# Optimization experiments

Measured on AMD Instinct MI355X. Metric: run time of the kernel, lower is better.

Reference implementation:

```python
import jax, jax.numpy as jnp
import numpy as np

N_NODES = 50000
N_EDGES = 800000
N_GRAPHS = 512
F_IN = 9
U = 64  # model_units


def _add_self_loops(edge_index, n):
    loop = jnp.arange(n, dtype=edge_index.dtype)
    return jnp.concatenate([edge_index, jnp.stack([loop, loop])], axis=1)


def gat_conv(x, edge_index, W, a_src, a_dst, b):
    # PyG GATConv, heads=1, negative_slope=0.2, add_self_loops=True
    n = x.shape[0]
    ei = _add_self_loops(edge_index, n)
    src, dst = ei[0], ei[1]
    h = x @ W                              # [n, U]
    alpha_s = h @ a_src                    # [n]
    alpha_d = h @ a_dst                    # [n]
    e = jax.nn.leaky_relu(alpha_s[src] + alpha_d[dst], 0.2)   # [E+n]
    m = jax.ops.segment_max(e, dst, num_segments=n)           # stable softmax over incoming edges
    ex = jnp.exp(e - m[dst])
    denom = jax.ops.segment_sum(ex, dst, num_segments=n)
    coef = ex / denom[dst]                 # [E+n]
    out = jax.ops.segment_sum(h[src] * coef[:, None], dst, num_segments=n)
    return out + b


def gcn_conv(x, edge_index, W, b):
    # PyG GCNConv with symmetric normalization and self loops
    n = x.shape[0]
    ei = _add_self_loops(edge_index, n)
    src, dst = ei[0], ei[1]
    h = x @ W                              # [n, U]
    deg = jax.ops.segment_sum(jnp.ones(src.shape, h.dtype), dst, num_segments=n)
    dinv = jnp.where(deg > 0, jax.lax.rsqrt(deg), 0.0)
    norm = dinv[src] * dinv[dst]           # [E+n]
    out = jax.ops.segment_sum(h[src] * norm[:, None], dst, num_segments=n)
    return out + b


def _branch(x, edge_index, W_gat, a_src, a_dst, b_gat, W_gcn, b_gcn, W1, b1, W2, b2, W3, b3):
    x = jnp.tanh(gat_conv(x, edge_index, W_gat, a_src, a_dst, b_gat))
    for i in range(W_gcn.shape[0]):        # model_layers - 1 = 2 GCN layers
        x = jnp.tanh(gcn_conv(x, edge_index, W_gcn[i], b_gcn[i]))
        # dropout is a no-op in eval mode
    x = jnp.tanh(x @ W1 + b1)
    x = jnp.tanh(x @ W2 + b2)
    x = x @ W3 + b3                        # [n, 1]; dropout no-op in eval
    return x


def _mean_pool(x, batch, num_graphs):
    sums = jax.ops.segment_sum(x, batch, num_segments=num_graphs)
    cnt = jax.ops.segment_sum(jnp.ones((x.shape[0],), x.dtype), batch, num_segments=num_graphs)
    return sums / jnp.maximum(cnt, 1.0)[:, None]


def setup_inputs() -> dict:
    key = jax.random.key(0)
    ks = jax.random.split(key, 16)
    inp = {
        "x_a": jax.random.normal(ks[0], (N_NODES, F_IN), jnp.float32),
        "x_b": jax.random.normal(ks[1], (N_NODES, F_IN), jnp.float32),
        "edge_index_a": jax.random.randint(ks[2], (2, N_EDGES), 0, N_NODES, jnp.int32),
        "edge_index_b": jax.random.randint(ks[3], (2, N_EDGES), 0, N_NODES, jnp.int32),
        "batch_a": jnp.sort(jax.random.randint(ks[4], (N_NODES,), 0, N_GRAPHS, jnp.int32)),
        "batch_b": jnp.sort(jax.random.randint(ks[5], (N_NODES,), 0, N_GRAPHS, jnp.int32)),
        # parameters
        "W_gat": jax.random.normal(ks[6], (F_IN, U), jnp.float32) * 0.3,
        "a_src": jax.random.normal(ks[7], (U,), jnp.float32) * 0.3,
        "a_dst": jax.random.normal(ks[8], (U,), jnp.float32) * 0.3,
        "b_gat": jnp.zeros((U,), jnp.float32),
        "W_gcn": jax.random.normal(ks[9], (2, U, U), jnp.float32) * (1.0 / np.sqrt(U)),
        "b_gcn": jnp.zeros((2, U), jnp.float32),
        "W1": jax.random.normal(ks[10], (U, U), jnp.float32) * (1.0 / np.sqrt(U)),
        "b1": jnp.zeros((U,), jnp.float32),
        "W2": jax.random.normal(ks[11], (U, 32), jnp.float32) * (1.0 / np.sqrt(U)),
        "b2": jnp.zeros((32,), jnp.float32),
        "W3": jax.random.normal(ks[12], (32, 1), jnp.float32) * (1.0 / np.sqrt(32.0)),
        "b3": jnp.zeros((1,), jnp.float32),
    }
    return inp


def reference(x_a, x_b, edge_index_a, edge_index_b, batch_a, batch_b,
              W_gat, a_src, a_dst, b_gat, W_gcn, b_gcn, W1, b1, W2, b2, W3, b3):
    params = (W_gat, a_src, a_dst, b_gat, W_gcn, b_gcn, W1, b1, W2, b2, W3, b3)
    ha = _branch(x_a, edge_index_a, *params)
    hb = _branch(x_b, edge_index_b, *params)
    ua = _mean_pool(ha, batch_a, N_GRAPHS)   # [G, 1]
    ub = _mean_pool(hb, batch_b, N_GRAPHS)
    return jax.nn.sigmoid(ub - ua)
```

## Files before the change

### kernel.cpp

```cpp
#include <hip/hip_runtime.h>
#include <hip/hip_fp16.h>
#include <math.h>

#define NN 50000
#define NE 800000
#define NG 512
#define NET (NE + NN)
#define NT2 ((2 * NN + 63) / 64)
#define GN4 ((2 * NN + 3) / 4)
#define GN8 ((2 * NN + 7) / 8)
#define GN32 ((2 * NN + 31) / 32)
#define NSH 68

#define SLICE 512
#define NSL ((NN + SLICE - 1) / SLICE)
#define CHK 4096
#define NCK ((NET + CHK - 1) / CHK)
#define CAP 10240

typedef unsigned short u16;

__device__ __forceinline__ float wsum64(float v) {
#pragma unroll
    for (int o = 32; o > 0; o >>= 1) v += __shfl_down(v, o, 64);
    return v;
}

__device__ __forceinline__ float fast_tanh(float x) {
    return 1.f - 2.f / (__expf(2.f * x) + 1.f);
}


__global__ __launch_bounds__(256) void k_hist(const int* __restrict__ eia,
                                              const int* __restrict__ eib,
                                              int* __restrict__ cnts) {
    __shared__ int h[NSL];
    int b = blockIdx.x;
    int br = b >= NCK, c = b - (br ? NCK : 0);
    int t = threadIdx.x;
    for (int i = t; i < NSL; i += 256) h[i] = 0;
    __syncthreads();
    const int* ei = br ? eib : eia;
    int e0 = c * CHK, e1 = e0 + CHK; if (e1 > NET) e1 = NET;
    for (int e = e0 + t; e < e1; e += 256) {
        int d = (e < NE) ? __builtin_nontemporal_load(&ei[NE + e]) : (e - NE);
        atomicAdd(&h[d >> 9], 1);
    }
    __syncthreads();
    for (int i = t; i < NSL; i += 256) cnts[(br * NSL + i) * NCK + c] = h[i];
}

__global__ __launch_bounds__(64) void k_off1(int* __restrict__ cnts,
                                             int* __restrict__ sliceBase) {
    int b = blockIdx.x;
    int br = b >= NSL, s = b - (br ? NSL : 0);
    int lane = threadIdx.x;
    int* row = cnts + (br * NSL + s) * NCK;
    int run = 0;
    for (int c0 = 0; c0 < NCK; c0 += 64) {
        int c = c0 + lane;
        int v = (c < NCK) ? row[c] : 0;
        int orig = v;
#pragma unroll
        for (int o = 1; o < 64; o <<= 1) {
            int tv = __shfl_up(v, o, 64);
            if (lane >= o) v += tv;
        }
        if (c < NCK) row[c] = run + v - orig;
        run += __shfl(v, 63, 64);
    }
    if (lane == 0) sliceBase[br * (NSL + 1) + s] = run;
}

__global__ void k_off2(int* __restrict__ sliceBase, int* __restrict__ rowptr2,
                       float* __restrict__ pool) {
    int t = threadIdx.x;
    for (int i = t; i < 4 * NG; i += 256) pool[i] = 0.f;
    if (t < 2) {
        int* sb = sliceBase + t * (NSL + 1);
        int run = 0;
        for (int s = 0; s < NSL; s++) { int v = sb[s]; sb[s] = run; run += v; }
        sb[NSL] = run;
        rowptr2[t * (NN + 1) + NN] = run;
    }
}

__global__ __launch_bounds__(256) void k_bucket(const int* __restrict__ eia,
                                                const int* __restrict__ eib,
                                                const int* __restrict__ cnts,
                                                const int* __restrict__ sliceBase,
                                                unsigned int* __restrict__ staging) {
    __shared__ int cur[NSL];
    int b = blockIdx.x;
    int br = b >= NCK, c = b - (br ? NCK : 0);
    int t = threadIdx.x;
    for (int i = t; i < NSL; i += 256)
        cur[i] = cnts[(br * NSL + i) * NCK + c] + sliceBase[br * (NSL + 1) + i];
    __syncthreads();
    const int* ei = br ? eib : eia;
    unsigned int* stg = staging + (size_t)br * NET;
    int e0 = c * CHK, e1 = e0 + CHK; if (e1 > NET) e1 = NET;
    for (int e = e0 + t; e < e1; e += 256) {
        int d, s;
        if (e < NE) {
            d = __builtin_nontemporal_load(&ei[NE + e]);
            s = __builtin_nontemporal_load(&ei[e]);
        } else { d = e - NE; s = d; }
        int pos = atomicAdd(&cur[d >> 9], 1);
        stg[pos] = ((unsigned int)(d & 511) << 16) | (unsigned int)s;
    }
}

__global__ __launch_bounds__(512) void k_slice(const unsigned int* __restrict__ staging,
                                               const int* __restrict__ sliceBase,
                                               int* __restrict__ rowptr2,
                                               float* __restrict__ dinv2,
                                               u16* __restrict__ csr2) {
    __shared__ int sc[512];
    __shared__ int cur[512];
    __shared__ u16 buf[CAP];
    int b = blockIdx.x;
    int br = b >= NSL, sl = b - (br ? NSL : 0);
    int t = threadIdx.x;
    const int* sb = sliceBase + br * (NSL + 1);
    int base = sb[sl], m = sb[sl + 1] - base;
    const unsigned int* st = staging + (size_t)br * NET + base;
    cur[t] = 0;
    __syncthreads();
    for (int i = t; i < m; i += 512) atomicAdd(&cur[st[i] >> 16], 1);
    __syncthreads();
    int v = cur[t];
    sc[t] = v;
    __syncthreads();
    for (int o = 1; o < 512; o <<= 1) {
        int add = (t >= o) ? sc[t - o] : 0;
        __syncthreads();
        sc[t] += add;
        __syncthreads();
    }
    int excl = sc[t] - v;
    int node = sl * SLICE + t;
    if (node < NN) {
        rowptr2[br * (NN + 1) + node] = base + excl;
        dinv2[br * NN + node] = v > 0 ? rsqrtf((float)v) : 0.f;
    }
    cur[t] = excl;
    __syncthreads();
    for (int i = t; i < m; i += 512) {
        unsigned int e = st[i];
        int pos = atomicAdd(&cur[e >> 16], 1);
        if (pos < CAP) buf[pos] = (u16)(e & 0xffffu);
    }
    __syncthreads();
    u16* out = csr2 + (size_t)br * NET + base;
    int mm = m < CAP ? m : CAP;
    for (int i = t; i < mm; i += 512) out[i] = buf[i];
}

__global__ __launch_bounds__(256) void k_wprep(const float* __restrict__ W1,
                                               const float* __restrict__ W2,
                                               const float* __restrict__ Wgcn,
                                               __half* __restrict__ out) {
    int i = blockIdx.x * 256 + threadIdx.x;
    float v;
    if (i < 4096) v = W1[i];
    else if (i < 6144) v = W2[i - 4096];
    else v = Wgcn[i - 6144];
    out[i] = __float2half(v);
}


__global__ void k_gat_input(const float* __restrict__ xa, const float* __restrict__ xb,
                            const float* __restrict__ Wg,
                            const float* __restrict__ avs, const float* __restrict__ avd,
                            __half* __restrict__ A, float* __restrict__ als,
                            float* __restrict__ ald) {
    __shared__ float sW[9 * 64];
    __shared__ float sas[64], sad[64];
    int t = threadIdx.x;
    for (int i = t; i < 9 * 64; i += 256) sW[i] = Wg[i];
    if (t < 64) { sas[t] = avs[t]; sad[t] = avd[t]; }
    __syncthreads();
    int n = blockIdx.x * 4 + (t >> 6);
    int u = t & 63;
    if (n >= 2 * NN) return;
    const float* xp = (n < NN) ? &xa[(size_t)n * 9] : &xb[(size_t)(n - NN) * 9];
    float h = 0.f;
#pragma unroll
    for (int f = 0; f < 9; f++) h += xp[f] * sW[f * 64 + u];
    A[(size_t)n * 64 + u] = __float2half(h);
    float ps = wsum64(h * sas[u]);
    float pd = wsum64(h * sad[u]);
    if (u == 0) { als[n] = ps; ald[n] = pd; }
}

__global__ __launch_bounds__(256) void k_edgew(
        const int* __restrict__ rowptr2, const u16* __restrict__ csr2,
        const float* __restrict__ als, const float* __restrict__ ald,
        float* __restrict__ wn) {
    int u = threadIdx.x & 63;
    int lu = u & 31;
    int dg = blockIdx.x * 8 + (threadIdx.x >> 6) * 2 + (u >> 5);
    if (dg >= 2 * NN) return;
    int br = dg >= NN;
    int d = dg - br * NN;
    const int* rp = rowptr2 + br * (NN + 1);
    const u16* cs = csr2 + br * NET;
    float* wp = wn + (size_t)br * NET;
    int nb = br * NN;
    int beg = rp[d], end = rp[d + 1];
    float ad = ald[dg];
    float den = 0.f;
    for (int c = beg + lu; c < end; c += 32) {
        int s = nb + cs[c];
        float v = als[s] + ad;
        float w = __expf(fmaxf(v, 0.2f * v));
        den += w;
        wp[c] = w;
    }
#pragma unroll
    for (int o = 16; o > 0; o >>= 1) den += __shfl_down(den, o, 32);
    den = __shfl(den, 0, 32);
    float inv = 1.f / den;
    for (int c = beg + lu; c < end; c += 32) wp[c] *= inv;
}

__device__ __forceinline__ void fma8(float* acc, float4 f, float w) {
    const __half2* h = (const __half2*)&f;
#pragma unroll
    for (int p = 0; p < 4; p++) {
        float2 v = __half22float2(h[p]);
        acc[2 * p]     += v.x * w;
        acc[2 * p + 1] += v.y * w;
    }
}

__global__ __launch_bounds__(256) void k_gat_gather8(
        const int* __restrict__ rowptr2, const u16* __restrict__ csr2,
        const float* __restrict__ wn, const __half* __restrict__ A,
        const float* __restrict__ bias, __half* __restrict__ B) {
    int lane = threadIdx.x & 63;
    int grp = lane >> 3, li = lane & 7;
    int dg = blockIdx.x * 32 + (threadIdx.x >> 6) * 8 + grp;
    int br = dg >= NN;
    int d = dg - br * NN;
    const int* rp = rowptr2 + br * (NN + 1);
    const u16* cs = csr2 + br * NET;
    const float* wp = wn + (size_t)br * NET;
    int nb = br * NN;
    int beg = rp[d], end = rp[d + 1];
    const float4* Af = (const float4*)A;
    float acc[8];
#pragma unroll
    for (int k = 0; k < 8; k++) acc[k] = 0.f;
    for (int j = beg; j < end; j += 4) {
        int i0 = j, i1 = j + 1, i2 = j + 2, i3 = j + 3;
        int c1 = i1 < end ? i1 : end - 1;
        int c2 = i2 < end ? i2 : end - 1;
        int c3 = i3 < end ? i3 : end - 1;
        float w0 = wp[i0];
        float w1 = i1 < end ? wp[c1] : 0.f;
        float w2 = i2 < end ? wp[c2] : 0.f;
        float w3 = i3 < end ? wp[c3] : 0.f;
        int s0 = nb + cs[i0];
        int s1 = nb + cs[c1];
        int s2 = nb + cs[c2];
        int s3 = nb + cs[c3];
        float4 f0 = Af[(size_t)s0 * 8 + li];
        float4 f1 = Af[(size_t)s1 * 8 + li];
        float4 f2 = Af[(size_t)s2 * 8 + li];
        float4 f3 = Af[(size_t)s3 * 8 + li];
        fma8(acc, f0, w0);
        fma8(acc, f1, w1);
        fma8(acc, f2, w2);
        fma8(acc, f3, w3);
    }
    const float4* bf = (const float4*)bias;
    float4 b0 = bf[2 * li], b1 = bf[2 * li + 1];
    __half2 o[4];
    o[0] = __floats2half2_rn(fast_tanh(acc[0] + b0.x), fast_tanh(acc[1] + b0.y));
    o[1] = __floats2half2_rn(fast_tanh(acc[2] + b0.z), fast_tanh(acc[3] + b0.w));
    o[2] = __floats2half2_rn(fast_tanh(acc[4] + b1.x), fast_tanh(acc[5] + b1.y));
    o[3] = __floats2half2_rn(fast_tanh(acc[6] + b1.z), fast_tanh(acc[7] + b1.w));
    ((float4*)B)[(size_t)dg * 8 + li] = *(float4*)o;
}

__global__ __launch_bounds__(256) void k_gcn_gather8(
        const int* __restrict__ rowptr2, const u16* __restrict__ csr2,
        const float* __restrict__ dinv, const __half* __restrict__ Y,
        const float* __restrict__ bias, __half* __restrict__ Bout) {
    int lane = threadIdx.x & 63;
    int grp = lane >> 3, li = lane & 7;
    int dg = blockIdx.x * 32 + (threadIdx.x >> 6) * 8 + grp;
    int br = dg >= NN;
    int d = dg - br * NN;
    const int* rp = rowptr2 + br * (NN + 1);
    const u16* cs = csr2 + br * NET;
    int nb = br * NN;
    int beg = rp[d], end = rp[d + 1];
    const float4* Yf = (const float4*)Y;
    float acc[8];
#pragma unroll
    for (int k = 0; k < 8; k++) acc[k] = 0.f;
    for (int j = beg; j < end; j += 4) {
        int i1 = j + 1, i2 = j + 2, i3 = j + 3;
        int c1 = i1 < end ? i1 : end - 1;
        int c2 = i2 < end ? i2 : end - 1;
        int c3 = i3 < end ? i3 : end - 1;
        float w1 = i1 < end ? 1.f : 0.f;
        float w2 = i2 < end ? 1.f : 0.f;
        float w3 = i3 < end ? 1.f : 0.f;
        int s0 = nb + cs[j];
        int s1 = nb + cs[c1];
        int s2 = nb + cs[c2];
        int s3 = nb + cs[c3];
        float4 f0 = Yf[(size_t)s0 * 8 + li];
        float4 f1 = Yf[(size_t)s1 * 8 + li];
        float4 f2 = Yf[(size_t)s2 * 8 + li];
        float4 f3 = Yf[(size_t)s3 * 8 + li];
        fma8(acc, f0, 1.f);
        fma8(acc, f1, w1);
        fma8(acc, f2, w2);
        fma8(acc, f3, w3);
    }
    float dv = dinv[dg];
    const float4* bf = (const float4*)bias;
    float4 b0 = bf[2 * li], b1 = bf[2 * li + 1];
    __half2 o[4];
    o[0] = __floats2half2_rn(fast_tanh(acc[0] * dv + b0.x), fast_tanh(acc[1] * dv + b0.y));
    o[1] = __floats2half2_rn(fast_tanh(acc[2] * dv + b0.z), fast_tanh(acc[3] * dv + b0.w));
    o[2] = __floats2half2_rn(fast_tanh(acc[4] * dv + b1.x), fast_tanh(acc[5] * dv + b1.y));
    o[3] = __floats2half2_rn(fast_tanh(acc[6] * dv + b1.z), fast_tanh(acc[7] * dv + b1.w));
    ((float4*)Bout)[(size_t)dg * 8 + li] = *(float4*)o;
}

__device__ __forceinline__ void load_tile_FM16(const __half* __restrict__ X, int base,
                                               __half* sXh, int t) {
    const float4* Xf = (const float4*)X;
#pragma unroll
    for (int rep = 0; rep < 2; rep++) {
        int i = t + rep * 256;
        int node = i >> 3, q = i & 7;
        float4 raw;
        if (base + node < 2 * NN) raw = Xf[(size_t)(base + node) * 8 + q];
        else raw = make_float4(0.f, 0.f, 0.f, 0.f);
        const __half* hv = (const __half*)&raw;
#pragma unroll
        for (int e = 0; e < 8; e++) sXh[(8 * q + e) * NSH + node] = hv[e];
    }
}

__global__ __launch_bounds__(256) void k_lin_tile(
        const __half* __restrict__ X, const __half* __restrict__ Wh,
        const float* __restrict__ dinv, __half* __restrict__ Y) {
    __shared__ __half sW[64 * 64];
    __shared__ __half sXh[64 * NSH];
    int t = threadIdx.x;
    {
        const uint4* src = (const uint4*)Wh;
        uint4* dst = (uint4*)sW;
        for (int i = t; i < 512; i += 256) dst[i] = src[i];
    }
    int base = blockIdx.x * 64;
    load_tile_FM16(X, base, sXh, t);
    __syncthreads();
    int tx = t & 15, ty = t >> 4;
    float acc[4][4];
#pragma unroll
    for (int i = 0; i < 4; i++)
#pragma unroll
        for (int j = 0; j < 4; j++) acc[i][j] = 0.f;
#pragma unroll 4
    for (int k = 0; k < 64; k++) {
        uint2 wraw = *(const uint2*)&sW[k * 64 + 4 * tx];
        float2 wa = __half22float2(*(__half2*)&wraw.x);
        float2 wb = __half22float2(*(__half2*)&wraw.y);
        uint2 xraw = *(const uint2*)&sXh[k * NSH + 4 * ty];
        float2 xa = __half22float2(*(__half2*)&xraw.x);
        float2 xb = __half22float2(*(__half2*)&xraw.y);
        acc[0][0] += xa.x * wa.x; acc[0][1] += xa.x * wa.y; acc[0][2] += xa.x * wb.x; acc[0][3] += xa.x * wb.y;
        acc[1][0] += xa.y * wa.x; acc[1][1] += xa.y * wa.y; acc[1][2] += xa.y * wb.x; acc[1][3] += xa.y * wb.y;
        acc[2][0] += xb.x * wa.x; acc[2][1] += xb.x * wa.y; acc[2][2] += xb.x * wb.x; acc[2][3] += xb.x * wb.y;
        acc[3][0] += xb.y * wa.x; acc[3][1] += xb.y * wa.y; acc[3][2] += xb.y * wb.x; acc[3][3] += xb.y * wb.y;
    }
#pragma unroll
    for (int i = 0; i < 4; i++) {
        int n = base + 4 * ty + i;
        if (n < 2 * NN) {
            float dv = dinv[n];
            __half2* Y2 = (__half2*)&Y[(size_t)n * 64 + 4 * tx];
            Y2[0] = __floats2half2_rn(acc[i][0] * dv, acc[i][1] * dv);
            Y2[1] = __floats2half2_rn(acc[i][2] * dv, acc[i][3] * dv);
        }
    }
}

__global__ __launch_bounds__(256) void k_mlp_pool(
        const __half* __restrict__ X,
        const int* __restrict__ batch_a, const int* __restrict__ batch_b,
        const __half* __restrict__ W1h, const float* __restrict__ b1,
        const __half* __restrict__ W2h, const float* __restrict__ b2,
        const float* __restrict__ W3, const float* __restrict__ b3,
        float* __restrict__ pool) {
    __shared__ __half sW1[64 * 64];
    __shared__ __half sW2[64 * 32];
    __shared__ __half sXh[64 * NSH];
    __shared__ float sP[64 * 9];
    __shared__ float sW3[32], sb1[64], sb2[32];
    __shared__ int sKey[64];
    __shared__ float sVal[64];
    int t = threadIdx.x;
    {
        const uint4* s1 = (const uint4*)W1h;
        uint4* d1 = (uint4*)sW1;
        for (int i = t; i < 512; i += 256) d1[i] = s1[i];
        const uint4* s2 = (const uint4*)W2h;
        uint4* d2 = (uint4*)sW2;
        if (t < 256) d2[t] = s2[t];
    }
    if (t < 64) sb1[t] = b1[t];
    if (t < 32) { sW3[t] = W3[t]; sb2[t] = b2[t]; }
    float bb3 = b3[0];
    int base = blockIdx.x * 64;
    load_tile_FM16(X, base, sXh, t);
    __syncthreads();
    int tx = t & 15, ty = t >> 4;
    float acc[4][4];
#pragma unroll
    for (int i = 0; i < 4; i++)
#pragma unroll
        for (int j = 0; j < 4; j++) acc[i][j] = sb1[4 * tx + j];
#pragma unroll 4
    for (int k = 0; k < 64; k++) {
        uint2 wraw = *(const uint2*)&sW1[k * 64 + 4 * tx];
        float2 wa = __half22float2(*(__half2*)&wraw.x);
        float2 wb = __half22float2(*(__half2*)&wraw.y);
        uint2 xraw = *(const uint2*)&sXh[k * NSH + 4 * ty];
        float2 xa = __half22float2(*(__half2*)&xraw.x);
        float2 xb = __half22float2(*(__half2*)&xraw.y);
        acc[0][0] += xa.x * wa.x; acc[0][1] += xa.x * wa.y; acc[0][2] += xa.x * wb.x; acc[0][3] += xa.x * wb.y;
        acc[1][0] += xa.y * wa.x; acc[1][1] += xa.y * wa.y; acc[1][2] += xa.y * wb.x; acc[1][3] += xa.y * wb.y;
        acc[2][0] += xb.x * wa.x; acc[2][1] += xb.x * wa.y; acc[2][2] += xb.x * wb.x; acc[2][3] += xb.x * wb.y;
        acc[3][0] += xb.y * wa.x; acc[3][1] += xb.y * wa.y; acc[3][2] += xb.y * wb.x; acc[3][3] += xb.y * wb.y;
    }
    __syncthreads();
#pragma unroll
    for (int j = 0; j < 4; j++) {
        __half2 h01 = __floats2half2_rn(fast_tanh(acc[0][j]), fast_tanh(acc[1][j]));
        __half2 h23 = __floats2half2_rn(fast_tanh(acc[2][j]), fast_tanh(acc[3][j]));
        uint2 packed = make_uint2(*(unsigned int*)&h01, *(unsigned int*)&h23);
        *(uint2*)&sXh[(4 * tx + j) * NSH + 4 * ty] = packed;
    }
    __syncthreads();
    int tx2 = t & 7, ty2 = t >> 3;
    float a2_[2][4];
#pragma unroll
    for (int i = 0; i < 2; i++)
#pragma unroll
        for (int j = 0; j < 4; j++) a2_[i][j] = sb2[4 * tx2 + j];
#pragma unroll 4
    for (int k = 0; k < 64; k++) {
        uint2 wraw = *(const uint2*)&sW2[k * 32 + 4 * tx2];
        float2 wa = __half22float2(*(__half2*)&wraw.x);
        float2 wb = __half22float2(*(__half2*)&wraw.y);
        unsigned int xraw = *(const unsigned int*)&sXh[k * NSH + 2 * ty2];
        float2 xv = __half22float2(*(__half2*)&xraw);
        a2_[0][0] += xv.x * wa.x; a2_[0][1] += xv.x * wa.y; a2_[0][2] += xv.x * wb.x; a2_[0][3] += xv.x * wb.y;
        a2_[1][0] += xv.y * wa.x; a2_[1][1] += xv.y * wa.y; a2_[1][2] += xv.y * wb.x; a2_[1][3] += xv.y * wb.y;
    }
#pragma unroll
    for (int i = 0; i < 2; i++) {
        float p = fast_tanh(a2_[i][0]) * sW3[4 * tx2]
                + fast_tanh(a2_[i][1]) * sW3[4 * tx2 + 1]
                + fast_tanh(a2_[i][2]) * sW3[4 * tx2 + 2]
                + fast_tanh(a2_[i][3]) * sW3[4 * tx2 + 3];
        sP[(2 * ty2 + i) * 9 + tx2] = p;
    }
    __syncthreads();
    if (t < 64) {
        int n = base + t;
        bool valid = n < 2 * NN;
        int br = n >= NN;
        int g = valid ? (br ? batch_b[n - NN] : batch_a[n]) : -1;
        int key = valid ? (br * 4096 + g) : -1;
        float s0 = sP[t * 9 + 0] + sP[t * 9 + 1] + sP[t * 9 + 2] + sP[t * 9 + 3];
        float s1 = sP[t * 9 + 4] + sP[t * 9 + 5] + sP[t * 9 + 6] + sP[t * 9 + 7];
        sKey[t] = key;
        sVal[t] = s0 + s1 + bb3;
        if (valid && (t == 0 || sKey[t - 1] != key)) {
            float sum = 0.f;
            int cnt = 0;
            for (int j = t; j < 64 && sKey[j] == key; j++) { sum += sVal[j]; cnt++; }
            float* bin = pool + br * 2 * NG;
            atomicAdd(&bin[g], sum);
            atomicAdd(&bin[NG + g], (float)cnt);
        }
    }
}

__global__ void k_final(const float* __restrict__ pool, float* __restrict__ out) {
    int g = blockIdx.x * 256 + threadIdx.x;
    if (g >= NG) return;
    float ua = pool[g] / fmaxf(pool[NG + g], 1.f);
    float ub = pool[2 * NG + g] / fmaxf(pool[3 * NG + g], 1.f);
    float z = ub - ua;
    out[g] = 1.f / (1.f + __expf(-z));
}

extern "C" void kernel_launch(void* const* d_in, const int* in_sizes, int n_in,
                              void* d_out, int out_size, void* d_ws, size_t ws_size,
                              hipStream_t stream) {
    const float* x_a = (const float*)d_in[0];
    const float* x_b = (const float*)d_in[1];
    const int* ei_a = (const int*)d_in[2];
    const int* ei_b = (const int*)d_in[3];
    const int* batch_a = (const int*)d_in[4];
    const int* batch_b = (const int*)d_in[5];
    const float* Wg   = (const float*)d_in[6];
    const float* avs  = (const float*)d_in[7];
    const float* avd  = (const float*)d_in[8];
    const float* bg   = (const float*)d_in[9];
    const float* Wgcn = (const float*)d_in[10];
    const float* bgcn = (const float*)d_in[11];
    const float* W1 = (const float*)d_in[12];
    const float* b1 = (const float*)d_in[13];
    const float* W2 = (const float*)d_in[14];
    const float* b2 = (const float*)d_in[15];
    const float* W3 = (const float*)d_in[16];
    const float* b3 = (const float*)d_in[17];

    char* w = (char*)d_ws;
    __half* A2 = (__half*)w;          w += (size_t)2 * NN * 64 * 2;
    __half* B2 = (__half*)w;          w += (size_t)2 * NN * 64 * 2;
    float* als2 = (float*)w;          w += (size_t)2 * NN * 4;
    float* ald2 = (float*)w;          w += (size_t)2 * NN * 4;
    float* dinv2 = (float*)w;         w += (size_t)2 * NN * 4;
    float* pool = (float*)w;          w += (size_t)4 * NG * 4;
    int* rowptr2 = (int*)w;           w += (size_t)2 * (NN + 1) * 4;
    int* cnts = (int*)w;              w += (size_t)2 * NSL * NCK * 4;
    int* sliceBase = (int*)w;         w += (size_t)2 * (NSL + 1) * 4;
    u16* csr2 = (u16*)w;              w += (size_t)2 * NET * 2;
    float* wn = (float*)w;            w += (size_t)2 * NET * 4;
    __half* wcache = (__half*)w;      w += (size_t)14336 * 2;
    unsigned int* staging = (unsigned int*)A2;

    __half* W1h = wcache;
    __half* W2h = wcache + 4096;
    __half* Wg0h = wcache + 6144;
    __half* Wg1h = wcache + 10240;

    dim3 blk(256);

    k_hist<<<2 * NCK, blk, 0, stream>>>(ei_a, ei_b, cnts);
    k_wprep<<<56, blk, 0, stream>>>(W1, W2, Wgcn, wcache);
    k_off1<<<2 * NSL, dim3(64), 0, stream>>>(cnts, sliceBase);
    k_off2<<<1, blk, 0, stream>>>(sliceBase, rowptr2, pool);
    k_bucket<<<2 * NCK, blk, 0, stream>>>(ei_a, ei_b, cnts, sliceBase, staging);
    k_slice<<<2 * NSL, dim3(512), 0, stream>>>(staging, sliceBase, rowptr2, dinv2, csr2);

    k_gat_input<<<GN4, blk, 0, stream>>>(x_a, x_b, Wg, avs, avd, A2, als2, ald2);
    k_edgew<<<GN8, blk, 0, stream>>>(rowptr2, csr2, als2, ald2, wn);
    k_gat_gather8<<<GN32, blk, 0, stream>>>(rowptr2, csr2, wn, A2, bg, B2);
    k_lin_tile<<<NT2, blk, 0, stream>>>(B2, Wg0h, dinv2, A2);
    k_gcn_gather8<<<GN32, blk, 0, stream>>>(rowptr2, csr2, dinv2, A2, bgcn, B2);
    k_lin_tile<<<NT2, blk, 0, stream>>>(B2, Wg1h, dinv2, A2);
    k_gcn_gather8<<<GN32, blk, 0, stream>>>(rowptr2, csr2, dinv2, A2, bgcn + 64, B2);
    k_mlp_pool<<<NT2, blk, 0, stream>>>(B2, batch_a, batch_b, W1h, b1, W2h, b2, W3, b3, pool);

    k_final<<<(NG + 255) / 256, blk, 0, stream>>>(pool, (float*)d_out);
}
```

Baseline: 354.6 us.

## Use MFMA f16 matrix instructions for dense linear and MLP tiles

Replaces the scalar FMA-based 64x64 tile matmuls in the GCN linear kernel and the MLP/pool kernel with 16x16x32 f16 MFMA intrinsics, storing weights pre-transposed in row-major shared tiles with padded stride. The weight-prep kernel now writes transposed fp16 weights. The final per-node dot with W3 uses a width-16 shuffle reduction instead of shared-memory partial sums. This reduces ALU instruction count in the dense stages, but adds scattered 2-byte global stores in the lin kernel output.

Measured after the change: 304.4 us (median of 2 runs). 14.2% less time.

```diff
diff --git a/kernel.cpp b/kernel.cpp
--- a/kernel.cpp
+++ b/kernel.cpp
@@ -10,7 +10,7 @@
 #define GN4 ((2 * NN + 3) / 4)
 #define GN8 ((2 * NN + 7) / 8)
 #define GN32 ((2 * NN + 31) / 32)
-#define NSH 68
+#define TS 72
 
 #define SLICE 512
 #define NSL ((NN + SLICE - 1) / SLICE)
@@ -19,6 +19,8 @@
 #define CAP 10240
 
 typedef unsigned short u16;
+typedef _Float16 h8 __attribute__((ext_vector_type(8)));
+typedef float f32x4 __attribute__((ext_vector_type(4)));
 
 __device__ __forceinline__ float wsum64(float v) {
 #pragma unroll
@@ -163,9 +165,10 @@
                                                __half* __restrict__ out) {
     int i = blockIdx.x * 256 + threadIdx.x;
     float v;
-    if (i < 4096) v = W1[i];
-    else if (i < 6144) v = W2[i - 4096];
-    else v = Wgcn[i - 6144];
+    if (i < 4096)       { int n = i >> 6,        k = i & 63; v = W1[k * 64 + n]; }
+    else if (i < 6144)  { int j = i - 4096; int n = j >> 6, k = j & 63; v = W2[k * 32 + n]; }
+    else if (i < 10240) { int j = i - 6144; int n = j >> 6, k = j & 63; v = Wgcn[k * 64 + n]; }
+    else                { int j = i - 10240; int n = j >> 6, k = j & 63; v = Wgcn[4096 + k * 64 + n]; }
     out[i] = __float2half(v);
 }
 
@@ -334,63 +337,49 @@
     ((float4*)Bout)[(size_t)dg * 8 + li] = *(float4*)o;
 }
 
-__device__ __forceinline__ void load_tile_FM16(const __half* __restrict__ X, int base,
-                                               __half* sXh, int t) {
+__global__ __launch_bounds__(256) void k_lin_tile(
+        const __half* __restrict__ X, const __half* __restrict__ Wt,
+        const float* __restrict__ dinv, __half* __restrict__ Y) {
+    __shared__ __half sX[64 * TS];
+    __shared__ __half sW[64 * TS];
+    int t = threadIdx.x;
+    int base = blockIdx.x * 64;
     const float4* Xf = (const float4*)X;
+    const float4* Wf = (const float4*)Wt;
 #pragma unroll
     for (int rep = 0; rep < 2; rep++) {
         int i = t + rep * 256;
-        int node = i >> 3, q = i & 7;
-        float4 raw;
-        if (base + node < 2 * NN) raw = Xf[(size_t)(base + node) * 8 + q];
-        else raw = make_float4(0.f, 0.f, 0.f, 0.f);
-        const __half* hv = (const __half*)&raw;
-#pragma unroll
-        for (int e = 0; e < 8; e++) sXh[(8 * q + e) * NSH + node] = hv[e];
-    }
-}
-
-__global__ __launch_bounds__(256) void k_lin_tile(
-        const __half* __restrict__ X, const __half* __restrict__ Wh,
-        const float* __restrict__ dinv, __half* __restrict__ Y) {
-    __shared__ __half sW[64 * 64];
-    __shared__ __half sXh[64 * NSH];
-    int t = threadIdx.x;
-    {
-        const uint4* src = (const uint4*)Wh;
-        uint4* dst = (uint4*)sW;
-        for (int i = t; i < 512; i += 256) dst[i] = src[i];
-    }
-    int base = blockIdx.x * 64;
-    load_tile_FM16(X, base, sXh, t);
-    __syncthreads();
-    int tx = t & 15, ty = t >> 4;
-    float acc[4][4];
-#pragma unroll
-    for (int i = 0; i < 4; i++)
-#pragma unroll
-        for (int j = 0; j < 4; j++) acc[i][j] = 0.f;
-#pragma unroll 4
-    for (int k = 0; k < 64; k++) {
-        uint2 wraw = *(const uint2*)&sW[k * 64 + 4 * tx];
-        float2 wa = __half22float2(*(__half2*)&wraw.x);
-        float2 wb = __half22float2(*(__half2*)&wraw.y);
-        uint2 xraw = *(const uint2*)&sXh[k * NSH + 4 * ty];
-        float2 xa = __half22float2(*(__half2*)&xraw.x);
-        float2 xb = __half22float2(*(__half2*)&xraw.y);
-        acc[0][0] += xa.x * wa.x; acc[0][1] += xa.x * wa.y; acc[0][2] += xa.x * wb.x; acc[0][3] += xa.x * wb.y;
-        acc[1][0] += xa.y * wa.x; acc[1][1] += xa.y * wa.y; acc[1][2] += xa.y * wb.x; acc[1][3] += xa.y * wb.y;
-        acc[2][0] += xb.x * wa.x; acc[2][1] += xb.x * wa.y; acc[2][2] += xb.x * wb.x; acc[2][3] += xb.x * wb.y;
-        acc[3][0] += xb.y * wa.x; acc[3][1] += xb.y * wa.y; acc[3][2] += xb.y * wb.x; acc[3][3] += xb.y * wb.y;
-    }
-#pragma unroll
-    for (int i = 0; i < 4; i++) {
-        int n = base + 4 * ty + i;
-        if (n < 2 * NN) {
-            float dv = dinv[n];
-            __half2* Y2 = (__half2*)&Y[(size_t)n * 64 + 4 * tx];
-            Y2[0] = __floats2half2_rn(acc[i][0] * dv, acc[i][1] * dv);
-            Y2[1] = __floats2half2_rn(acc[i][2] * dv, acc[i][3] * dv);
+        int row = i >> 3, q = i & 7;
+        *(float4*)&sW[row * TS + q * 8] = Wf[i];
+        float4 x;
+        if (base + row < 2 * NN) x = Xf[(size_t)(base + row) * 8 + q];
+        else x = make_float4(0.f, 0.f, 0.f, 0.f);
+        *(float4*)&sX[row * TS + q * 8] = x;
+    }
+    __syncthreads();
+    int l = t & 63, w = t >> 6;
+    int lr = l & 15, lg = l >> 4;
+    h8 av0 = *(const h8*)&sX[(16 * w + lr) * TS + 8 * lg];
+    h8 av1 = *(const h8*)&sX[(16 * w + lr) * TS + 32 + 8 * lg];
+    f32x4 acc[4];
+#pragma unroll
+    for (int s = 0; s < 4; s++) {
+        h8 bv0 = *(const h8*)&sW[(16 * s + lr) * TS + 8 * lg];
+        h8 bv1 = *(const h8*)&sW[(16 * s + lr) * TS + 32 + 8 * lg];
+        f32x4 c = {0.f, 0.f, 0.f, 0.f};
+        c = __builtin_amdgcn_mfma_f32_16x16x32_f16(av0, bv0, c, 0, 0, 0);
+        c = __builtin_amdgcn_mfma_f32_16x16x32_f16(av1, bv1, c, 0, 0, 0);
+        acc[s] = c;
+    }
+    int nrow = base + 16 * w + 4 * lg;
+    float4 dv4 = *(const float4*)&dinv[16 * w + 4 * lg + base];
+#pragma unroll
+    for (int s = 0; s < 4; s++) {
+        int col = 16 * s + lr;
+#pragma unroll
+        for (int i = 0; i < 4; i++) {
+            int n = nrow + i;
+            if (n < 2 * NN) Y[(size_t)n * 64 + col] = __float2half(acc[s][i] * dv4[i]);
         }
     }
 }
@@ -398,83 +387,86 @@
 __global__ __launch_bounds__(256) void k_mlp_pool(
         const __half* __restrict__ X,
         const int* __restrict__ batch_a, const int* __restrict__ batch_b,
-        const __half* __restrict__ W1h, const float* __restrict__ b1,
-        const __half* __restrict__ W2h, const float* __restrict__ b2,
+        const __half* __restrict__ W1t, const float* __restrict__ b1,
+        const __half* __restrict__ W2t, const float* __restrict__ b2,
         const float* __restrict__ W3, const float* __restrict__ b3,
         float* __restrict__ pool) {
-    __shared__ __half sW1[64 * 64];
-    __shared__ __half sW2[64 * 32];
-    __shared__ __half sXh[64 * NSH];
-    __shared__ float sP[64 * 9];
-    __shared__ float sW3[32], sb1[64], sb2[32];
+    __shared__ __half sX[64 * TS];
+    __shared__ __half sW1[64 * TS];
+    __shared__ __half sW2[32 * TS];
+    __shared__ float sP[64];
     __shared__ int sKey[64];
     __shared__ float sVal[64];
     int t = threadIdx.x;
+    int base = blockIdx.x * 64;
+    const float4* Xf = (const float4*)X;
+    const float4* W1f = (const float4*)W1t;
+    const float4* W2f = (const float4*)W2t;
+#pragma unroll
+    for (int rep = 0; rep < 2; rep++) {
+        int i = t + rep * 256;
+        int row = i >> 3, q = i & 7;
+        *(float4*)&sW1[row * TS + q * 8] = W1f[i];
+        float4 x;
+        if (base + row < 2 * NN) x = Xf[(size_t)(base + row) * 8 + q];
+        else x = make_float4(0.f, 0.f, 0.f, 0.f);
+        *(float4*)&sX[row * TS + q * 8] = x;
+    }
     {
-        const uint4* s1 = (const uint4*)W1h;
-        uint4* d1 = (uint4*)sW1;
-        for (int i = t; i < 512; i += 256) d1[i] = s1[i];
-        const uint4* s2 = (const uint4*)W2h;
-        uint4* d2 = (uint4*)sW2;
-        if (t < 256) d2[t] = s2[t];
-    }
-    if (t < 64) sb1[t] = b1[t];
-    if (t < 32) { sW3[t] = W3[t]; sb2[t] = b2[t]; }
+        int row = t >> 3, q = t & 7;
+        *(float4*)&sW2[row * TS + q * 8] = W2f[t];
+    }
     float bb3 = b3[0];
-    int base = blockIdx.x * 64;
-    load_tile_FM16(X, base, sXh, t);
-    __syncthreads();
-    int tx = t & 15, ty = t >> 4;
-    float acc[4][4];
+    __syncthreads();
+    int l = t & 63, w = t >> 6;
+    int lr = l & 15, lg = l >> 4;
+    h8 av0 = *(const h8*)&sX[(16 * w + lr) * TS + 8 * lg];
+    h8 av1 = *(const h8*)&sX[(16 * w + lr) * TS + 32 + 8 * lg];
+    f32x4 d1[4];
+#pragma unroll
+    for (int s = 0; s < 4; s++) {
+        float bias = b1[16 * s + lr];
+        f32x4 c = {bias, bias, bias, bias};
+        h8 bv0 = *(const h8*)&sW1[(16 * s + lr) * TS + 8 * lg];
+        h8 bv1 = *(const h8*)&sW1[(16 * s + lr) * TS + 32 + 8 * lg];
+        c = __builtin_amdgcn_mfma_f32_16x16x32_f16(av0, bv0, c, 0, 0, 0);
+        c = __builtin_amdgcn_mfma_f32_16x16x32_f16(av1, bv1, c, 0, 0, 0);
+        d1[s] = c;
+    }
+#pragma unroll
+    for (int s = 0; s < 4; s++) {
+#pragma unroll
+        for (int i = 0; i < 4; i++) {
+            sX[(16 * w + 4 * lg + i) * TS + 16 * s + lr] = __float2half(fast_tanh(d1[s][i]));
+        }
+    }
+    __syncthreads();
+    h8 a20 = *(const h8*)&sX[(16 * w + lr) * TS + 8 * lg];
+    h8 a21 = *(const h8*)&sX[(16 * w + lr) * TS + 32 + 8 * lg];
+    f32x4 d2[2];
+#pragma unroll
+    for (int s = 0; s < 2; s++) {
+        float bias = b2[16 * s + lr];
+        f32x4 c = {bias, bias, bias, bias};
+        h8 bv0 = *(const h8*)&sW2[(16 * s + lr) * TS + 8 * lg];
+        h8 bv1 = *(const h8*)&sW2[(16 * s + lr) * TS + 32 + 8 * lg];
+        c = __builtin_amdgcn_mfma_f32_16x16x32_f16(a20, bv0, c, 0, 0, 0);
+        c = __builtin_amdgcn_mfma_f32_16x16x32_f16(a21, bv1, c, 0, 0, 0);
+        d2[s] = c;
+    }
+    float w3a = W3[lr], w3b = W3[16 + lr];
+    float pr[4];
 #pragma unroll
     for (int i = 0; i < 4; i++)
-#pragma unroll
-        for (int j = 0; j < 4; j++) acc[i][j] = sb1[4 * tx + j];
-#pragma unroll 4
-    for (int k = 0; k < 64; k++) {
-        uint2 wraw = *(const uint2*)&sW1[k * 64 + 4 * tx];
-        float2 wa = __half22float2(*(__half2*)&wraw.x);
-        float2 wb = __half22float2(*(__half2*)&wraw.y);
-        uint2 xraw = *(const uint2*)&sXh[k * NSH + 4 * ty];
-        float2 xa = __half22float2(*(__half2*)&xraw.x);
-        float2 xb = __half22float2(*(__half2*)&xraw.y);
-        acc[0][0] += xa.x * wa.x; acc[0][1] += xa.x * wa.y; acc[0][2] += xa.x * wb.x; acc[0][3] += xa.x * wb.y;
-        acc[1][0] += xa.y * wa.x; acc[1][1] += xa.y * wa.y; acc[1][2] += xa.y * wb.x; acc[1][3] += xa.y * wb.y;
-        acc[2][0] += xb.x * wa.x; acc[2][1] += xb.x * wa.y; acc[2][2] += xb.x * wb.x; acc[2][3] += xb.x * wb.y;
-        acc[3][0] += xb.y * wa.x; acc[3][1] += xb.y * wa.y; acc[3][2] += xb.y * wb.x; acc[3][3] += xb.y * wb.y;
-    }
-    __syncthreads();
-#pragma unroll
-    for (int j = 0; j < 4; j++) {
-        __half2 h01 = __floats2half2_rn(fast_tanh(acc[0][j]), fast_tanh(acc[1][j]));
-        __half2 h23 = __floats2half2_rn(fast_tanh(acc[2][j]), fast_tanh(acc[3][j]));
-        uint2 packed = make_uint2(*(unsigned int*)&h01, *(unsigned int*)&h23);
-        *(uint2*)&sXh[(4 * tx + j) * NSH + 4 * ty] = packed;
-    }
-    __syncthreads();
-    int tx2 = t & 7, ty2 = t >> 3;
-    float a2_[2][4];
-#pragma unroll
-    for (int i = 0; i < 2; i++)
-#pragma unroll
-        for (int j = 0; j < 4; j++) a2_[i][j] = sb2[4 * tx2 + j];
-#pragma unroll 4
-    for (int k = 0; k < 64; k++) {
-        uint2 wraw = *(const uint2*)&sW2[k * 32 + 4 * tx2];
-        float2 wa = __half22float2(*(__half2*)&wraw.x);
-        float2 wb = __half22float2(*(__half2*)&wraw.y);
-        unsigned int xraw = *(const unsigned int*)&sXh[k * NSH + 2 * ty2];
-        float2 xv = __half22float2(*(__half2*)&xraw);
-        a2_[0][0] += xv.x * wa.x; a2_[0][1] += xv.x * wa.y; a2_[0][2] += xv.x * wb.x; a2_[0][3] += xv.x * wb.y;
-        a2_[1][0] += xv.y * wa.x; a2_[1][1] += xv.y * wa.y; a2_[1][2] += xv.y * wb.x; a2_[1][3] += xv.y * wb.y;
-    }
-#pragma unroll
-    for (int i = 0; i < 2; i++) {
-        float p = fast_tanh(a2_[i][0]) * sW3[4 * tx2]
-                + fast_tanh(a2_[i][1]) * sW3[4 * tx2 + 1]
-                + fast_tanh(a2_[i][2]) * sW3[4 * tx2 + 2]
-                + fast_tanh(a2_[i][3]) * sW3[4 * tx2 + 3];
-        sP[(2 * ty2 + i) * 9 + tx2] = p;
+        pr[i] = fast_tanh(d2[0][i]) * w3a + fast_tanh(d2[1][i]) * w3b;
+#pragma unroll
+    for (int o = 1; o < 16; o <<= 1) {
+#pragma unroll
+        for (int i = 0; i < 4; i++) pr[i] += __shfl_xor(pr[i], o, 16);
+    }
+    if (lr == 0) {
+#pragma unroll
+        for (int i = 0; i < 4; i++) sP[16 * w + 4 * lg + i] = pr[i];
     }
     __syncthreads();
     if (t < 64) {
@@ -483,10 +475,9 @@
         int br = n >= NN;
         int g = valid ? (br ? batch_b[n - NN] : batch_a[n]) : -1;
         int key = valid ? (br * 4096 + g) : -1;
-        float s0 = sP[t * 9 + 0] + sP[t * 9 + 1] + sP[t * 9 + 2] + sP[t * 9 + 3];
-        float s1 = sP[t * 9 + 4] + sP[t * 9 + 5] + sP[t * 9 + 6] + sP[t * 9 + 7];
         sKey[t] = key;
-        sVal[t] = s0 + s1 + bb3;
+        sVal[t] = sP[t] + bb3;
+        __builtin_amdgcn_s_barrier();
         if (valid && (t == 0 || sKey[t - 1] != key)) {
             float sum = 0.f;
             int cnt = 0;
@@ -544,10 +535,10 @@
     __half* wcache = (__half*)w;      w += (size_t)14336 * 2;
     unsigned int* staging = (unsigned int*)A2;
 
-    __half* W1h = wcache;
-    __half* W2h = wcache + 4096;
-    __half* Wg0h = wcache + 6144;
-    __half* Wg1h = wcache + 10240;
+    __half* W1t = wcache;
+    __half* W2t = wcache + 4096;
+    __half* Wg0t = wcache + 6144;
+    __half* Wg1t = wcache + 10240;
 
     dim3 blk(256);
 
@@ -561,11 +552,11 @@
     k_gat_input<<<GN4, blk, 0, stream>>>(x_a, x_b, Wg, avs, avd, A2, als2, ald2);
     k_edgew<<<GN8, blk, 0, stream>>>(rowptr2, csr2, als2, ald2, wn);
     k_gat_gather8<<<GN32, blk, 0, stream>>>(rowptr2, csr2, wn, A2, bg, B2);
-    k_lin_tile<<<NT2, blk, 0, stream>>>(B2, Wg0h, dinv2, A2);
+    k_lin_tile<<<NT2, blk, 0, stream>>>(B2, Wg0t, dinv2, A2);
     k_gcn_gather8<<<GN32, blk, 0, stream>>>(rowptr2, csr2, dinv2, A2, bgcn, B2);
-    k_lin_tile<<<NT2, blk, 0, stream>>>(B2, Wg1h, dinv2, A2);
+    k_lin_tile<<<NT2, blk, 0, stream>>>(B2, Wg1t, dinv2, A2);
     k_gcn_gather8<<<GN32, blk, 0, stream>>>(rowptr2, csr2, dinv2, A2, bgcn + 64, B2);
-    k_mlp_pool<<<NT2, blk, 0, stream>>>(B2, batch_a, batch_b, W1h, b1, W2h, b2, W3, b3, pool);
+    k_mlp_pool<<<NT2, blk, 0, stream>>>(B2, batch_a, batch_b, W1t, b1, W2t, b2, W3, b3, pool);
 
     k_final<<<(NG + 255) / 256, blk, 0, stream>>>(pool, (float*)d_out);
 }
```
